# Optimization experiments

Hardware: AMD Instinct MI355X
Metric: run time of the kernel (lower is better)

The kernel has to match this reference:

```python
import jax, jax.numpy as jnp
import numpy as np
import math

B, S, D, H, DFF = 4, 1024, 1024, 16, 4096
DK = D // H
EPS = 1e-5


def setup_inputs() -> dict:
    key = jax.random.key(0)
    ks = jax.random.split(key, 20)
    n = lambda k, shp: jax.random.normal(k, shp, jnp.float32) * 0.02
    inp = {
        "x": jax.random.normal(ks[0], (B, S, D), jnp.float32),
        "enc_output": jax.random.normal(ks[1], (B, S, D), jnp.float32),
        # source_mask is unused by the module's forward; target_mask is causal
        "source_mask": jnp.ones((B, 1, 1, S), jnp.int32),
        "target_mask": jnp.tril(jnp.ones((1, 1, S, S), jnp.int32)),
        # self-attention (torch Linear: y = x @ W.T + b)
        "sa_wq": n(ks[2], (D, D)), "sa_bq": jnp.zeros((D,), jnp.float32),
        "sa_wk": n(ks[3], (D, D)), "sa_bk": jnp.zeros((D,), jnp.float32),
        "sa_wv": n(ks[4], (D, D)), "sa_bv": jnp.zeros((D,), jnp.float32),
        "sa_wo": n(ks[5], (D, D)), "sa_bo": jnp.zeros((D,), jnp.float32),
        # cross-attention (nn.MultiheadAttention packed in_proj)
        "ca_in_w": n(ks[6], (3 * D, D)), "ca_in_b": jnp.zeros((3 * D,), jnp.float32),
        "ca_out_w": n(ks[7], (D, D)), "ca_out_b": jnp.zeros((D,), jnp.float32),
        # feed-forward
        "ff_w1": n(ks[8], (DFF, D)), "ff_b1": jnp.zeros((DFF,), jnp.float32),
        "ff_w2": n(ks[9], (D, DFF)), "ff_b2": jnp.zeros((D,), jnp.float32),
        # layer norms
        "n1_g": jnp.ones((D,), jnp.float32), "n1_b": jnp.zeros((D,), jnp.float32),
        "n2_g": jnp.ones((D,), jnp.float32), "n2_b": jnp.zeros((D,), jnp.float32),
        "n3_g": jnp.ones((D,), jnp.float32), "n3_b": jnp.zeros((D,), jnp.float32),
    }
    return inp


def _layernorm(x, g, b):
    m = jnp.mean(x, axis=-1, keepdims=True)
    v = jnp.var(x, axis=-1, keepdims=True)
    return (x - m) * jax.lax.rsqrt(v + EPS) * g + b


def _split_heads(t):  # [B,L,D] -> [B,H,L,DK]
    Bb, L, _ = t.shape
    return t.reshape(Bb, L, H, DK).transpose(0, 2, 1, 3)


def _attn(q, k, v, mask):
    # q,k,v: [B,H,Lq/ Lk, DK]
    scores = jnp.einsum("bhqd,bhkd->bhqk", q, k) / math.sqrt(DK)
    if mask is not None:
        scores = jnp.where(mask == 0, jnp.float32(-1e9), scores)
    probs = jax.nn.softmax(scores, axis=-1)
    out = jnp.einsum("bhqk,bhkd->bhqd", probs, v)  # [B,H,Lq,DK]
    Bb, _, Lq, _ = out.shape
    return out.transpose(0, 2, 1, 3).reshape(Bb, Lq, D)


def reference(x, enc_output, source_mask, target_mask,
              sa_wq, sa_bq, sa_wk, sa_bk, sa_wv, sa_bv, sa_wo, sa_bo,
              ca_in_w, ca_in_b, ca_out_w, ca_out_b,
              ff_w1, ff_b1, ff_w2, ff_b2,
              n1_g, n1_b, n2_g, n2_b, n3_g, n3_b):
    # --- masked causal self-attention (hand-rolled MultiHeadAttention) ---
    q = _split_heads(x @ sa_wq.T + sa_bq)
    k = _split_heads(x @ sa_wk.T + sa_bk)
    v = _split_heads(x @ sa_wv.T + sa_bv)
    sa = _attn(q, k, v, target_mask) @ sa_wo.T + sa_bo
    x = _layernorm(x + sa, n1_g, n1_b)  # dropout p=0 -> identity

    # --- cross-attention (nn.MultiheadAttention, batch_first, no mask) ---
    wq, wk, wv = ca_in_w[:D], ca_in_w[D:2 * D], ca_in_w[2 * D:]
    bq, bk, bv = ca_in_b[:D], ca_in_b[D:2 * D], ca_in_b[2 * D:]
    q = _split_heads(x @ wq.T + bq)
    k = _split_heads(enc_output @ wk.T + bk)
    v = _split_heads(enc_output @ wv.T + bv)
    ca = _attn(q, k, v, None) @ ca_out_w.T + ca_out_b
    x = _layernorm(x + ca, n2_g, n2_b)

    # --- feed-forward ---
    ff = jax.nn.relu(x @ ff_w1.T + ff_b1) @ ff_w2.T + ff_b2
    x = _layernorm(x + ff, n3_g, n3_b)
    return x
```

## Files before the change

### kernel.cpp

```cpp
#include <hip/hip_runtime.h>
#include <hip/hip_bf16.h>
#include <stdint.h>
#include <math.h>

#define DEV static __device__ __forceinline__

typedef short bf16x8 __attribute__((ext_vector_type(8)));
typedef float f32x4 __attribute__((ext_vector_type(4)));
typedef float f32x16 __attribute__((ext_vector_type(16)));
typedef unsigned short u16;

static constexpr int Sq   = 1024;
static constexpr int Dm   = 1024;
static constexpr int Hh   = 16;
static constexpr int Mrows = 4096;
static constexpr int DFFn = 4096;


DEV u16 f2bf(float f) {
    union { float f; unsigned u; } c; c.f = f;
    unsigned u = c.u;
    return (u16)((u + 0x7FFFu + ((u >> 16) & 1u)) >> 16);
}

DEV float bf2f(u16 v) {
    union { unsigned u; float f; } c; c.u = ((unsigned)v) << 16; return c.f;
}

DEV unsigned cvt_pk_bf16(float lo, float hi) {
    unsigned r;
    asm("v_cvt_pk_bf16_f32 %0, %1, %2" : "=v"(r) : "v"(lo), "v"(hi));
    return r;
}

DEV float fast_exp2(float x) {
#if __has_builtin(__builtin_amdgcn_exp2f)
    return __builtin_amdgcn_exp2f(x);
#else
    float r; asm("v_exp_f32 %0, %1" : "=v"(r) : "v"(x)); return r;
#endif
}

DEV void gload_lds16(void* lds, const void* g) {
    using gvp = __attribute__((address_space(1))) void*;
    using lvp = __attribute__((address_space(3))) void*;
    __builtin_amdgcn_global_load_lds((gvp)const_cast<void*>(g), (lvp)lds, 16, 0, 0);
}

DEV int swz64(int L) { return L ^ (((L >> 7) & 7) << 4); }


__global__ __launch_bounds__(256) void cast_multi_kernel(
    const float* s0, const float* s1, const float* s2, const float* s3, const float* s4,
    const float* s5, const float* s6, const float* s7, const float* s8, const float* s9,
    u16* d0, u16* d1, u16* d2, u16* d3, u16* d4,
    u16* d5, u16* d6, u16* d7, u16* d8, u16* d9,
    int e0, int e1, int e2, int e3, int e4,
    int e5, int e6, int e7, int e8, int e9)
{
    int i = blockIdx.x * 256 + threadIdx.x;
    if (i >= e9) return;
    const float* s; u16* d; int b;
    if      (i < e0) { s = s0; d = d0; b = 0;  }
    else if (i < e1) { s = s1; d = d1; b = e0; }
    else if (i < e2) { s = s2; d = d2; b = e1; }
    else if (i < e3) { s = s3; d = d3; b = e2; }
    else if (i < e4) { s = s4; d = d4; b = e3; }
    else if (i < e5) { s = s5; d = d5; b = e4; }
    else if (i < e6) { s = s6; d = d6; b = e5; }
    else if (i < e7) { s = s7; d = d7; b = e6; }
    else if (i < e8) { s = s8; d = d8; b = e7; }
    else             { s = s9; d = d9; b = e8; }
    int j = i - b;
    float4 v = ((const float4*)s)[j];
    ushort4 o;
    o.x = f2bf(v.x); o.y = f2bf(v.y); o.z = f2bf(v.z); o.w = f2bf(v.w);
    ((ushort4*)d)[j] = o;
}


template<int MODE, int BSPLIT>
__global__ __launch_bounds__(512) void gemm256_kernel(
    const u16* __restrict__ A, const u16* __restrict__ W,
    const float* __restrict__ bias0, const float* __restrict__ bias1,
    const float* __restrict__ bias2,
    void* __restrict__ Cout,
    void* __restrict__ P1, void* __restrict__ P2, void* __restrict__ P3,
    int N, int ldK, int Kpass)
{
    __shared__ char ldsA[65536];
    __shared__ char ldsB[65536];
    const int tid = threadIdx.x;
    const int w = tid >> 6, l = tid & 63;
    const int lr = l & 15, lg = l >> 4;
    const int wr = w >> 2, wc = w & 3;

    const int nwg = gridDim.x * gridDim.y;
    const int lin = blockIdx.y * gridDim.x + blockIdx.x;
    const int swz = (lin & 7) * (nwg >> 3) + (lin >> 3);
    const size_t tm = (size_t)(swz / gridDim.x) * 256;
    const size_t tn = (size_t)(swz % gridDim.x) * 256;
    const size_t kz = (size_t)blockIdx.z * Kpass;

    int offA[8], offB[4];
    #pragma unroll
    for (int m = 0; m < 8; ++m)
        offA[m] = swz64((wr * 128 + m * 16 + lr) * 64 + lg * 16);
    #pragma unroll
    for (int n = 0; n < 4; ++n)
        offB[n] = swz64((wc * 64 + n * 16 + lr) * 64 + lg * 16);

    const int Ls = swz64(tid * 16);
    const int sr = Ls >> 6, scc = Ls & 63;
    const size_t ldb = (size_t)ldK * 2;
    const char* aS = (const char*)A + (tm + sr) * ldb + kz * 2 + scc;
    const char* bS = (const char*)W + (tn + sr) * ldb + kz * 2 + scc;

    auto AH = [&](int b, int h) -> char* { return ldsA + (b * 2 + h) * 16384; };
    auto BH = [&](int b, int h) -> char* { return ldsB + (b * 2 + h) * 16384; };
    auto stage = [&](char* half, const char* src) {
        gload_lds16(half + w * 1024, src);
        gload_lds16(half + 8192 + w * 1024, src + 128 * ldb);
    };

    const int nt = Kpass >> 6;
    const int niter = nt >> 1;

    f32x4 acc[8][4] = {};
    bf16x8 bq[4];

    stage(AH(0, 0), aS);        stage(BH(0, 0), bS);
    stage(AH(0, 1), aS + 64);   stage(BH(0, 1), bS + 64);
    stage(AH(1, 0), aS + 128);  stage(BH(1, 0), bS + 128);
    asm volatile("s_waitcnt vmcnt(4)" ::: "memory");
    __builtin_amdgcn_s_barrier();

    for (int it = 0; it < niter; ++it) {
        const int t0 = it * 2;
        const bool last = (it == niter - 1);
        #pragma unroll
        for (int p = 0; p < 8; ++p) {
            const int ts = p >> 2;
            const int kk = (p >> 1) & 1, mh = p & 1;

            if (mh == 0) {
                #pragma unroll
                for (int n = 0; n < 4; ++n)
                    bq[n] = *(const bf16x8*)(BH(ts, kk) + offB[n]);
            }
            bf16x8 aF[4];
            #pragma unroll
            for (int q = 0; q < 4; ++q)
                aF[q] = *(const bf16x8*)(AH(ts, kk) + offA[mh * 4 + q]);

            if (p == 0)      { stage(AH(1, 1), aS + (size_t)(t0 + 1) * 128 + 64); }
            else if (p == 1) { stage(BH(1, 1), bS + (size_t)(t0 + 1) * 128 + 64); }
            else if (p == 2) { if (t0 + 2 < nt) stage(AH(0, 0), aS + (size_t)(t0 + 2) * 128); }
            else if (p == 3) { if (t0 + 2 < nt) stage(BH(0, 0), bS + (size_t)(t0 + 2) * 128); }
            else if (p == 4) { if (t0 + 2 < nt) stage(AH(0, 1), aS + (size_t)(t0 + 2) * 128 + 64); }
            else if (p == 5) { if (t0 + 2 < nt) stage(BH(0, 1), bS + (size_t)(t0 + 2) * 128 + 64); }
            else if (p == 6) { if (t0 + 3 < nt) stage(AH(1, 0), aS + (size_t)(t0 + 3) * 128); }
            else             { if (t0 + 3 < nt) stage(BH(1, 0), bS + (size_t)(t0 + 3) * 128); }

            if (p == 3) {
                if (last) asm volatile("s_waitcnt vmcnt(0)" ::: "memory");
                else      asm volatile("s_waitcnt vmcnt(4)" ::: "memory");
            } else if (p == 7 && !last) {
                asm volatile("s_waitcnt vmcnt(4)" ::: "memory");
            }
            __builtin_amdgcn_s_barrier();
            asm volatile("s_waitcnt lgkmcnt(0)");
            __builtin_amdgcn_sched_barrier(0);
            __builtin_amdgcn_s_setprio(1);
            #pragma unroll
            for (int q = 0; q < 4; ++q)
                #pragma unroll
                for (int n = 0; n < 4; ++n)
                    acc[mh * 4 + q][n] = __builtin_amdgcn_mfma_f32_16x16x32_bf16(
                        aF[q], bq[n], acc[mh * 4 + q][n], 0, 0, 0);
            __builtin_amdgcn_s_setprio(0);
        }
    }

    u16* Pp = nullptr;
    float bv[4];
    if (MODE == 3) {
        Pp = (u16*)((blockIdx.z == 0) ? Cout : (blockIdx.z == 1) ? P1 : (blockIdx.z == 2) ? P2 : P3);
    } else {
        #pragma unroll
        for (int n = 0; n < 4; ++n) {
            const int col = (int)tn + wc * 64 + n * 16 + lr;
            if (BSPLIT) {
                const float* bp = (col < 1024) ? bias0 : (col < 2048) ? bias1 : bias2;
                bv[n] = bp[col & 1023];
            } else {
                bv[n] = bias0[col];
            }
        }
    }
    #pragma unroll
    for (int m = 0; m < 8; ++m) {
        #pragma unroll
        for (int n = 0; n < 4; ++n) {
            const size_t col = tn + wc * 64 + n * 16 + lr;
            #pragma unroll
            for (int j = 0; j < 4; ++j) {
                const size_t row = tm + wr * 128 + m * 16 + lg * 4 + j;
                if (MODE == 3) {
                    Pp[row * (size_t)N + col] = f2bf(acc[m][n][j]);
                } else {
                    float v = acc[m][n][j] + bv[n];
                    if (MODE == 2) v = fmaxf(v, 0.f);
                    ((u16*)Cout)[row * (size_t)N + col] = f2bf(v);
                }
            }
        }
    }
}


template<int OUT_BF16, int RELU, int BSPLIT>
__global__ __launch_bounds__(256, 3) void gemm_bt64_kernel(
    const u16* __restrict__ A, const u16* __restrict__ W,
    const float* __restrict__ bias0, const float* __restrict__ bias1,
    const float* __restrict__ bias2,
    void* __restrict__ Cout,
    int N, int K)
{
    __shared__ char Ald[2][8192];
    __shared__ char Bld[2][16384];
    const int tid = threadIdx.x;
    const int w  = tid >> 6, l = tid & 63;
    const int lr = l & 15,  lg = l >> 4;

    const int nwg = gridDim.x * gridDim.y;
    const int lin = blockIdx.y * gridDim.x + blockIdx.x;
    const int swz = (lin & 7) * (nwg >> 3) + (lin >> 3);
    const size_t tm = (size_t)(swz / gridDim.x) * 64;
    const size_t tn = (size_t)(swz % gridDim.x) * 128;

    const int Ls = swz64(tid * 16);
    const int sr = Ls >> 7, sc = (Ls & 127) >> 1;
    const u16* As = A + (tm + sr) * (size_t)K + sc;
    const u16* Bs = W + (tn + sr) * (size_t)K + sc;
    const int woff = w * 1024;

    auto stage = [&](int b, int k0) {
        gload_lds16(Ald[b] + woff,         As + k0);
        gload_lds16(Ald[b] + 4096 + woff,  As + (size_t)32 * K + k0);
        gload_lds16(Bld[b] + woff,         Bs + k0);
        gload_lds16(Bld[b] + 4096 + woff,  Bs + (size_t)32 * K + k0);
        gload_lds16(Bld[b] + 8192 + woff,  Bs + (size_t)64 * K + k0);
        gload_lds16(Bld[b] + 12288 + woff, Bs + (size_t)96 * K + k0);
    };

    int offA[4][2], offB[2][2];
    #pragma unroll
    for (int m = 0; m < 4; ++m)
        #pragma unroll
        for (int kk = 0; kk < 2; ++kk)
            offA[m][kk] = swz64((m * 16 + lr) * 128 + kk * 64 + lg * 16);
    #pragma unroll
    for (int n = 0; n < 2; ++n)
        #pragma unroll
        for (int kk = 0; kk < 2; ++kk)
            offB[n][kk] = swz64((w * 32 + n * 16 + lr) * 128 + kk * 64 + lg * 16);

    f32x4 acc[4][2] = {};
    const int nt = K >> 6;

    stage(0, 0);
    asm volatile("s_waitcnt vmcnt(0)" ::: "memory");
    __syncthreads();

    for (int t = 0; t < nt; ++t) {
        const int cur = t & 1;
        if (t + 1 < nt) stage(cur ^ 1, (t + 1) * 64);
        #pragma unroll
        for (int kk = 0; kk < 2; ++kk) {
            bf16x8 aF[4], bq[2];
            #pragma unroll
            for (int m = 0; m < 4; ++m) aF[m] = *(const bf16x8*)(Ald[cur] + offA[m][kk]);
            #pragma unroll
            for (int n = 0; n < 2; ++n) bq[n] = *(const bf16x8*)(Bld[cur] + offB[n][kk]);
            asm volatile("s_waitcnt lgkmcnt(0)");
            __builtin_amdgcn_sched_barrier(0);
            __builtin_amdgcn_s_setprio(1);
            #pragma unroll
            for (int m = 0; m < 4; ++m)
                #pragma unroll
                for (int n = 0; n < 2; ++n)
                    acc[m][n] = __builtin_amdgcn_mfma_f32_16x16x32_bf16(aF[m], bq[n], acc[m][n], 0, 0, 0);
            __builtin_amdgcn_s_setprio(0);
        }
        if (t + 1 < nt) asm volatile("s_waitcnt vmcnt(0)" ::: "memory");
        __syncthreads();
    }

    float bv[2];
    #pragma unroll
    for (int n = 0; n < 2; ++n) {
        const int col = (int)tn + w * 32 + n * 16 + lr;
        if (BSPLIT) {
            const float* bp = (col < 1024) ? bias0 : (col < 2048) ? bias1 : bias2;
            bv[n] = bp[col & 1023];
        } else {
            bv[n] = bias0[col];
        }
    }

    #pragma unroll
    for (int m = 0; m < 4; ++m) {
        #pragma unroll
        for (int n = 0; n < 2; ++n) {
            const size_t col = tn + w * 32 + n * 16 + lr;
            #pragma unroll
            for (int j = 0; j < 4; ++j) {
                const size_t row = tm + m * 16 + lg * 4 + j;
                float v = acc[m][n][j] + bv[n];
                if (RELU) v = fmaxf(v, 0.f);
                if (OUT_BF16) ((u16*)Cout)[row * (size_t)N + col] = f2bf(v);
                else          ((float*)Cout)[row * (size_t)N + col] = v;
            }
        }
    }
}


template<int CAUSAL>
__global__ __launch_bounds__(512, 2) void attn_kernel(
    const u16* __restrict__ Qm, int ldq,
    const u16* __restrict__ Km, int ldk,
    const u16* __restrict__ Vm, int ldv,
    u16* __restrict__ Om)
{
    __shared__ char lds[66048];

    const int tid = threadIdx.x;
    const int w = tid >> 6, l = tid & 63;
    const int lq = l & 31, hi = l >> 5;
    const int s = w & 3, hfk = w >> 2;
    const int bh = blockIdx.x;
    const int b = bh >> 4, h = bh & 15;
    const int q0 = (CAUSAL ? (gridDim.y - 1 - blockIdx.y) : blockIdx.y) * 128;
    const int qw0 = q0 + s * 32;
    const size_t baseQ = (size_t)b * Sq * ldq + (size_t)h * 64;
    const size_t baseK = (size_t)b * Sq * ldk + (size_t)h * 64;
    const size_t baseV = (size_t)b * Sq * ldv + (size_t)h * 64;
    const size_t baseO = (size_t)b * Sq * Dm  + (size_t)h * 64;

    const int qrow = qw0 + lq;
    bf16x8 bq[4];
    #pragma unroll
    for (int kc = 0; kc < 4; ++kc)
        bq[kc] = *(const bf16x8*)&Qm[baseQ + (size_t)qrow * ldq + kc * 16 + hi * 8];

    const int tl = tid & 255, pstg = tid >> 8;
    const int kr  = tl >> 2;
    const int kcB = (tl & 3) * 32;
    const int vdg = tl >> 5;
    const int vkp = tl & 31;

    f32x16 o0 = {}, o1 = {};
    float lj = 0.f;

    const int nt_blk  = CAUSAL ? ((q0 + 128) >> 6) : (Sq >> 6);
    const int nrounds = nt_blk >> 1;
    const float cexp = 0.125f * 1.44269504f;
    const float CSH  = 10.0f;

    uint4 ka, kb, va, vb;
    auto loadKV = [&](int rv) {
        const int kv = (rv * 2 + pstg) << 6;
        ka = *(const uint4*)&Km[baseK + (size_t)(kv + kr) * ldk + kcB / 2];
        kb = *(const uint4*)&Km[baseK + (size_t)(kv + kr) * ldk + kcB / 2 + 8];
        va = *(const uint4*)&Vm[baseV + (size_t)(kv + vkp * 2    ) * ldv + vdg * 8];
        vb = *(const uint4*)&Vm[baseV + (size_t)(kv + vkp * 2 + 1) * ldv + vdg * 8];
    };
    auto stageTo = [&](int bsel) {
        char* Kst = lds + bsel * 32768 + pstg * 8192;
        char* Vst = lds + bsel * 32768 + 16384 + pstg * 8192;
        const int sk = (kr & 7) << 4;
        *(uint4*)(Kst + kr * 128 + ((kcB     ) ^ sk)) = ka;
        *(uint4*)(Kst + kr * 128 + ((kcB + 16) ^ sk)) = kb;
        const u16* pa_ = (const u16*)&va;
        const u16* pb_ = (const u16*)&vb;
        #pragma unroll
        for (int i = 0; i < 8; ++i) {
            const int d = vdg * 8 + i;
            unsigned val = (unsigned)pa_[i] | ((unsigned)pb_[i] << 16);
            *(unsigned*)(Vst + d * 128 + ((vkp * 4) ^ ((d & 7) << 4))) = val;
        }
    };

    loadKV(0);
    stageTo(0);
    loadKV(1);
    __syncthreads();

    for (int r = 0; r < nrounds; ++r) {
        const int rp = r & 1;
        const char* Kb_ = lds + rp * 32768 + hfk * 8192;
        const char* Vb_ = lds + rp * 32768 + 16384 + hfk * 8192;
        const int kv0 = (r * 2 + hfk) << 6;
        const bool docmp = (!CAUSAL || kv0 < qw0 + 32);
        const int skq = (lq & 7) << 4;

        f32x16 sv[2];
        if (docmp) {
            sv[0] = (f32x16){}; sv[1] = (f32x16){};
            #pragma unroll
            for (int n = 0; n < 2; ++n) {
                const int rowb = (n * 32 + lq) * 128;
                #pragma unroll
                for (int kc = 0; kc < 4; ++kc) {
                    bf16x8 kf = *(const bf16x8*)(Kb_ + rowb + ((kc * 32 + hi * 16) ^ skq));
                    sv[n] = __builtin_amdgcn_mfma_f32_32x32x16_bf16(kf, bq[kc], sv[n], 0, 0, 0);
                }
            }
        }

        if (r + 1 < nrounds) stageTo(rp ^ 1);
        if (r + 2 < nrounds) loadKV(r + 2);

        if (docmp) {
            const bool diag = CAUSAL && (kv0 + 63 > qw0);
            float rs0 = 0.f, rs1 = 0.f;
            #pragma unroll
            for (int n = 0; n < 2; ++n)
                #pragma unroll
                for (int r2 = 0; r2 < 16; ++r2) {
                    float v = sv[n][r2];
                    if (diag) {
                        int key = kv0 + n * 32 + (r2 & 3) + 8 * (r2 >> 2) + 4 * hi;
                        if (key > qrow) v = -3.0e8f;
                    }
                    float e = fast_exp2(fmaf(v, cexp, -CSH));
                    sv[n][r2] = e;
                    if (r2 & 1) rs1 += e; else rs0 += e;
                }
            float rs = rs0 + rs1;
            rs += __shfl_xor(rs, 32);
            lj += rs;

            unsigned wv[2][8];
            #pragma unroll
            for (int n = 0; n < 2; ++n)
                #pragma unroll
                for (int m = 0; m < 8; ++m)
                    wv[n][m] = cvt_pk_bf16(sv[n][2 * m], sv[n][2 * m + 1]);

            #pragma unroll
            for (int ks = 0; ks < 4; ++ks) {
                const int n = ks >> 1, q_ = (ks & 1) * 4;
                unsigned r0 = (unsigned)__shfl_xor((int)wv[n][q_ + 0], 32);
                unsigned r1 = (unsigned)__shfl_xor((int)wv[n][q_ + 1], 32);
                unsigned r2w = (unsigned)__shfl_xor((int)wv[n][q_ + 2], 32);
                unsigned r3 = (unsigned)__shfl_xor((int)wv[n][q_ + 3], 32);
                union { unsigned u[4]; bf16x8 v; } pa;
                pa.u[0] = hi ? r2w           : wv[n][q_ + 0];
                pa.u[1] = hi ? r3            : wv[n][q_ + 1];
                pa.u[2] = hi ? wv[n][q_ + 2] : r0;
                pa.u[3] = hi ? wv[n][q_ + 3] : r1;
                const int koff = (ks * 32 + hi * 16);
                bf16x8 vf0 = *(const bf16x8*)(Vb_ + lq * 128        + (koff ^ skq));
                bf16x8 vf1 = *(const bf16x8*)(Vb_ + (32 + lq) * 128 + (koff ^ skq));
                o0 = __builtin_amdgcn_mfma_f32_32x32x16_bf16(pa.v, vf0, o0, 0, 0, 0);
                o1 = __builtin_amdgcn_mfma_f32_32x32x16_bf16(pa.v, vf1, o1, 0, 0, 0);
            }
        }
        __syncthreads();
    }

    char* ob = lds + s * 8192 + l * 128;
    float* mlb = (float*)(lds + 65536) + s * 32 + lq;
    const int sko = (l & 7) << 4;

    if (hfk == 1) {
        #pragma unroll
        for (int i = 0; i < 4; ++i) {
            f32x4 t0v = { o0[4 * i], o0[4 * i + 1], o0[4 * i + 2], o0[4 * i + 3] };
            f32x4 t1v = { o1[4 * i], o1[4 * i + 1], o1[4 * i + 2], o1[4 * i + 3] };
            *(f32x4*)(ob + ((i * 16) ^ sko))      = t0v;
            *(f32x4*)(ob + ((64 + i * 16) ^ sko)) = t1v;
        }
        if (hi == 0) mlb[0] = lj;
    }
    __syncthreads();
    if (hfk == 0) {
        const float linv = __builtin_amdgcn_rcpf(lj + mlb[0]);
        f32x4 b0[4], b1[4];
        #pragma unroll
        for (int i = 0; i < 4; ++i) {
            b0[i] = *(const f32x4*)(ob + ((i * 16) ^ sko));
            b1[i] = *(const f32x4*)(ob + ((64 + i * 16) ^ sko));
        }
        #pragma unroll
        for (int r2 = 0; r2 < 16; ++r2) {
            const int crow = (r2 & 3) + 8 * (r2 >> 2) + 4 * hi;
            const float lr_ = __shfl(linv, crow);
            const size_t rowoff = baseO + (size_t)(qw0 + crow) * Dm;
            float v0 = (o0[r2] + b0[r2 >> 2][r2 & 3]) * lr_;
            float v1 = (o1[r2] + b1[r2 >> 2][r2 & 3]) * lr_;
            Om[rowoff + lq]      = f2bf(v0);
            Om[rowoff + 32 + lq] = f2bf(v1);
        }
    }
}


__global__ __launch_bounds__(256) void add_ln_kernel(
    const u16* __restrict__ A, const u16* __restrict__ Bv,
    const float* __restrict__ g, const float* __restrict__ be,
    u16* __restrict__ Y)
{
    const int row = blockIdx.x;
    const int tid = threadIdx.x;
    const size_t off = (size_t)row * Dm;
    ushort4 a4 = ((const ushort4*)(A + off))[tid];
    ushort4 b4 = ((const ushort4*)(Bv + off))[tid];
    float4 xv;
    xv.x = bf2f(a4.x) + bf2f(b4.x);
    xv.y = bf2f(a4.y) + bf2f(b4.y);
    xv.z = bf2f(a4.z) + bf2f(b4.z);
    xv.w = bf2f(a4.w) + bf2f(b4.w);
    float s = xv.x + xv.y + xv.z + xv.w;
    float q = xv.x * xv.x + xv.y * xv.y + xv.z * xv.z + xv.w * xv.w;
    #pragma unroll
    for (int m = 1; m < 64; m <<= 1) {
        s += __shfl_xor(s, m);
        q += __shfl_xor(q, m);
    }
    __shared__ float ss[4], qq[4];
    if ((tid & 63) == 0) { ss[tid >> 6] = s; qq[tid >> 6] = q; }
    __syncthreads();
    s = ss[0] + ss[1] + ss[2] + ss[3];
    q = qq[0] + qq[1] + qq[2] + qq[3];
    const float mean = s * (1.f / 1024.f);
    const float var  = q * (1.f / 1024.f) - mean * mean;
    const float rstd = rsqrtf(var + 1e-5f);
    float4 g4  = ((const float4*)g)[tid];
    float4 be4 = ((const float4*)be)[tid];
    ushort4 ob;
    ob.x = f2bf((xv.x - mean) * rstd * g4.x + be4.x);
    ob.y = f2bf((xv.y - mean) * rstd * g4.y + be4.y);
    ob.z = f2bf((xv.z - mean) * rstd * g4.z + be4.z);
    ob.w = f2bf((xv.w - mean) * rstd * g4.w + be4.w);
    ((ushort4*)(Y + off))[tid] = ob;
}


__global__ __launch_bounds__(256) void add_ln_red4_kernel(
    const u16* __restrict__ X,
    const u16* __restrict__ P0, const u16* __restrict__ P1,
    const u16* __restrict__ P2, const u16* __restrict__ P3,
    const float* __restrict__ bias,
    const float* __restrict__ g, const float* __restrict__ be,
    float* __restrict__ Y)
{
    const int row = blockIdx.x;
    const int tid = threadIdx.x;
    const size_t off = (size_t)row * Dm;
    ushort4 a4 = ((const ushort4*)(X + off))[tid];
    ushort4 u0 = ((const ushort4*)(P0 + off))[tid];
    ushort4 u1 = ((const ushort4*)(P1 + off))[tid];
    ushort4 u2 = ((const ushort4*)(P2 + off))[tid];
    ushort4 u3 = ((const ushort4*)(P3 + off))[tid];
    float4 b4 = ((const float4*)bias)[tid];
    float4 xv;
    xv.x = bf2f(a4.x) + bf2f(u0.x) + bf2f(u1.x) + bf2f(u2.x) + bf2f(u3.x) + b4.x;
    xv.y = bf2f(a4.y) + bf2f(u0.y) + bf2f(u1.y) + bf2f(u2.y) + bf2f(u3.y) + b4.y;
    xv.z = bf2f(a4.z) + bf2f(u0.z) + bf2f(u1.z) + bf2f(u2.z) + bf2f(u3.z) + b4.z;
    xv.w = bf2f(a4.w) + bf2f(u0.w) + bf2f(u1.w) + bf2f(u2.w) + bf2f(u3.w) + b4.w;
    float s = xv.x + xv.y + xv.z + xv.w;
    float q = xv.x * xv.x + xv.y * xv.y + xv.z * xv.z + xv.w * xv.w;
    #pragma unroll
    for (int m = 1; m < 64; m <<= 1) {
        s += __shfl_xor(s, m);
        q += __shfl_xor(q, m);
    }
    __shared__ float ss[4], qq[4];
    if ((tid & 63) == 0) { ss[tid >> 6] = s; qq[tid >> 6] = q; }
    __syncthreads();
    s = ss[0] + ss[1] + ss[2] + ss[3];
    q = qq[0] + qq[1] + qq[2] + qq[3];
    const float mean = s * (1.f / 1024.f);
    const float var  = q * (1.f / 1024.f) - mean * mean;
    const float rstd = rsqrtf(var + 1e-5f);
    float4 g4  = ((const float4*)g)[tid];
    float4 be4 = ((const float4*)be)[tid];
    float4 y;
    y.x = (xv.x - mean) * rstd * g4.x + be4.x;
    y.y = (xv.y - mean) * rstd * g4.y + be4.y;
    y.z = (xv.z - mean) * rstd * g4.z + be4.z;
    y.w = (xv.w - mean) * rstd * g4.w + be4.w;
    ((float4*)(Y + off))[tid] = y;
}


extern "C" void kernel_launch(void* const* d_in, const int* in_sizes, int n_in,
                              void* d_out, int out_size, void* d_ws, size_t ws_size,
                              hipStream_t stream)
{
    const float* x       = (const float*)d_in[0];
    const float* enc     = (const float*)d_in[1];
    const float* sa_wq   = (const float*)d_in[4];
    const float* sa_bq   = (const float*)d_in[5];
    const float* sa_wk   = (const float*)d_in[6];
    const float* sa_bk   = (const float*)d_in[7];
    const float* sa_wv   = (const float*)d_in[8];
    const float* sa_bv   = (const float*)d_in[9];
    const float* sa_wo   = (const float*)d_in[10];
    const float* sa_bo   = (const float*)d_in[11];
    const float* ca_in_w = (const float*)d_in[12];
    const float* ca_in_b = (const float*)d_in[13];
    const float* ca_out_w= (const float*)d_in[14];
    const float* ca_out_b= (const float*)d_in[15];
    const float* ff_w1   = (const float*)d_in[16];
    const float* ff_b1   = (const float*)d_in[17];
    const float* ff_w2   = (const float*)d_in[18];
    const float* ff_b2   = (const float*)d_in[19];
    const float* n1_g = (const float*)d_in[20];
    const float* n1_b = (const float*)d_in[21];
    const float* n2_g = (const float*)d_in[22];
    const float* n2_b = (const float*)d_in[23];
    const float* n3_g = (const float*)d_in[24];
    const float* n3_b = (const float*)d_in[25];

    char* p = (char*)d_ws;
    auto take = [&](size_t bytes) -> char* {
        char* r = p; p += (bytes + 255) & ~(size_t)255; return r;
    };
    const size_t MDbf = (size_t)Mrows * Dm * 2;
    const size_t DD   = (size_t)Dm * Dm;

    u16* xb     = (u16*)take(MDbf);
    u16* encb   = (u16*)take(MDbf);
    u16* wqkv   = (u16*)take(3 * DD * 2);
    u16* wob    = (u16*)take(DD * 2);
    u16* cainb  = (u16*)take(3 * DD * 2);
    u16* caoutb = (u16*)take(DD * 2);
    u16* fw1b   = (u16*)take((size_t)DFFn * Dm * 2);
    u16* fw2b   = (u16*)take((size_t)Dm * DFFn * 2);
    u16* SCR    = (u16*)take((size_t)Mrows * DFFn * 2);
    u16* AOb    = (u16*)take(MDbf);
    u16* tmpb   = (u16*)take(MDbf);
    u16* x1bf   = (u16*)take(MDbf);
    u16* x2bf   = (u16*)take(MDbf);
    if ((size_t)(p - (char*)d_ws) > ws_size) return;

    u16* fp0 = AOb;
    u16* fp1 = tmpb;
    u16* fp2 = xb;
    u16* fp3 = encb;

    {
        const int sx  = (int)((size_t)Mrows * Dm / 4);
        const int sw  = (int)(DD / 4);
        const int e0 = sx;
        const int e1 = e0 + sx;
        const int e2 = e1 + sw;
        const int e3 = e2 + sw;
        const int e4 = e3 + sw;
        const int e5 = e4 + sw;
        const int e6 = e5 + 3 * sw;
        const int e7 = e6 + sw;
        const int e8 = e7 + 4 * sw;
        const int e9 = e8 + 4 * sw;
        cast_multi_kernel<<<dim3((e9 + 255) / 256), dim3(256), 0, stream>>>(
            x, enc, sa_wq, sa_wk, sa_wv, sa_wo, ca_in_w, ca_out_w, ff_w1, ff_w2,
            xb, encb, wqkv, wqkv + DD, wqkv + 2 * DD, wob, cainb, caoutb, fw1b, fw2b,
            e0, e1, e2, e3, e4, e5, e6, e7, e8, e9);
    }

    const dim3 blk(256);
    const dim3 blk512(512);
    const size_t M4 = (size_t)Mrows * Dm;

    gemm_bt64_kernel<1, 0, 1><<<dim3(3072 / 128, Mrows / 64), blk, 0, stream>>>(
        xb, wqkv, sa_bq, sa_bk, sa_bv, (void*)SCR, 3072, Dm);
    attn_kernel<1><<<dim3(4 * Hh, Sq / 128), blk512, 0, stream>>>(SCR, 3072, SCR + 1024, 3072, SCR + 2048, 3072, AOb);
    gemm_bt64_kernel<1, 0, 0><<<dim3(Dm / 128, Mrows / 64), blk, 0, stream>>>(
        AOb, wob, sa_bo, nullptr, nullptr, (void*)tmpb, Dm, Dm);
    add_ln_kernel<<<dim3(Mrows), blk, 0, stream>>>(xb, tmpb, n1_g, n1_b, x1bf);

    u16* Qc  = SCR;
    u16* KVc = SCR + M4;
    gemm_bt64_kernel<1, 0, 0><<<dim3(Dm / 128, Mrows / 64), blk, 0, stream>>>(
        x1bf, cainb, ca_in_b, nullptr, nullptr, (void*)Qc, Dm, Dm);
    gemm_bt64_kernel<1, 0, 0><<<dim3(2048 / 128, Mrows / 64), blk, 0, stream>>>(
        encb, cainb + DD, ca_in_b + Dm, nullptr, nullptr, (void*)KVc, 2048, Dm);
    attn_kernel<0><<<dim3(4 * Hh, Sq / 128), blk512, 0, stream>>>(Qc, 1024, KVc, 2048, KVc + 1024, 2048, AOb);
    gemm_bt64_kernel<1, 0, 0><<<dim3(Dm / 128, Mrows / 64), blk, 0, stream>>>(
        AOb, caoutb, ca_out_b, nullptr, nullptr, (void*)tmpb, Dm, Dm);
    add_ln_kernel<<<dim3(Mrows), blk, 0, stream>>>(x1bf, tmpb, n2_g, n2_b, x2bf);

    u16* ffh = SCR;
    gemm_bt64_kernel<1, 1, 0><<<dim3(DFFn / 128, Mrows / 64), blk, 0, stream>>>(
        x2bf, fw1b, ff_b1, nullptr, nullptr, (void*)ffh, DFFn, Dm);
    gemm256_kernel<3, 0><<<dim3(4, 16, 4), blk512, 0, stream>>>(
        ffh, fw2b, nullptr, nullptr, nullptr, (void*)fp0, (void*)fp1, (void*)fp2, (void*)fp3, Dm, DFFn, 1024);
    add_ln_red4_kernel<<<dim3(Mrows), blk, 0, stream>>>(x2bf, fp0, fp1, fp2, fp3, ff_b2, n3_g, n3_b, (float*)d_out);
}
```

Baseline: 310.0 us.

## Route QKV, cross-KV and FFN1 GEMMs through 256-tile kernel with split-K

```diff
diff --git a/kernel.cpp b/kernel.cpp
--- a/kernel.cpp
+++ b/kernel.cpp
@@ -76,6 +76,24 @@
     ushort4 o;
     o.x = f2bf(v.x); o.y = f2bf(v.y); o.z = f2bf(v.z); o.w = f2bf(v.w);
     ((ushort4*)d)[j] = o;
+}
+
+
+__global__ __launch_bounds__(256) void add2_bias_bf16_kernel(
+    const u16* __restrict__ P0, const u16* __restrict__ P1,
+    const float* __restrict__ bias, u16* __restrict__ Y, int N)
+{
+    const int i = blockIdx.x * 256 + threadIdx.x;
+    ushort4 a = ((const ushort4*)P0)[i];
+    ushort4 b = ((const ushort4*)P1)[i];
+    const int col = (i * 4) & (N - 1);
+    float4 bv = *(const float4*)&bias[col];
+    ushort4 o;
+    o.x = f2bf(bf2f(a.x) + bf2f(b.x) + bv.x);
+    o.y = f2bf(bf2f(a.y) + bf2f(b.y) + bv.y);
+    o.z = f2bf(bf2f(a.z) + bf2f(b.z) + bv.z);
+    o.w = f2bf(bf2f(a.w) + bf2f(b.w) + bv.w);
+    ((ushort4*)Y)[i] = o;
 }
 
 
@@ -647,12 +665,16 @@
     u16* tmpb   = (u16*)take(MDbf);
     u16* x1bf   = (u16*)take(MDbf);
     u16* x2bf   = (u16*)take(MDbf);
+    u16* cpbuf  = (u16*)take((size_t)Mrows * 2048 * 2);
     if ((size_t)(p - (char*)d_ws) > ws_size) return;
 
     u16* fp0 = AOb;
     u16* fp1 = tmpb;
     u16* fp2 = xb;
     u16* fp3 = encb;
+
+    u16* cp0 = cpbuf;
+    u16* cp1 = AOb;
 
     {
         const int sx  = (int)((size_t)Mrows * Dm / 4);
@@ -677,8 +699,8 @@
     const dim3 blk512(512);
     const size_t M4 = (size_t)Mrows * Dm;
 
-    gemm_bt64_kernel<1, 0, 1><<<dim3(3072 / 128, Mrows / 64), blk, 0, stream>>>(
-        xb, wqkv, sa_bq, sa_bk, sa_bv, (void*)SCR, 3072, Dm);
+    gemm256_kernel<1, 1><<<dim3(12, 16), blk512, 0, stream>>>(
+        xb, wqkv, sa_bq, sa_bk, sa_bv, (void*)SCR, nullptr, nullptr, nullptr, 3072, Dm, Dm);
     attn_kernel<1><<<dim3(4 * Hh, Sq / 128), blk512, 0, stream>>>(SCR, 3072, SCR + 1024, 3072, SCR + 2048, 3072, AOb);
     gemm_bt64_kernel<1, 0, 0><<<dim3(Dm / 128, Mrows / 64), blk, 0, stream>>>(
         AOb, wob, sa_bo, nullptr, nullptr, (void*)tmpb, Dm, Dm);
@@ -688,16 +710,19 @@
     u16* KVc = SCR + M4;
     gemm_bt64_kernel<1, 0, 0><<<dim3(Dm / 128, Mrows / 64), blk, 0, stream>>>(
         x1bf, cainb, ca_in_b, nullptr, nullptr, (void*)Qc, Dm, Dm);
-    gemm_bt64_kernel<1, 0, 0><<<dim3(2048 / 128, Mrows / 64), blk, 0, stream>>>(
-        encb, cainb + DD, ca_in_b + Dm, nullptr, nullptr, (void*)KVc, 2048, Dm);
+    gemm256_kernel<3, 0><<<dim3(8, 16, 2), blk512, 0, stream>>>(
+        encb, cainb + DD, nullptr, nullptr, nullptr,
+        (void*)cp0, (void*)cp1, nullptr, nullptr, 2048, Dm, 512);
+    add2_bias_bf16_kernel<<<dim3((Mrows * 2048 / 4) / 256), blk, 0, stream>>>(
+        cp0, cp1, ca_in_b + Dm, KVc, 2048);
     attn_kernel<0><<<dim3(4 * Hh, Sq / 128), blk512, 0, stream>>>(Qc, 1024, KVc, 2048, KVc + 1024, 2048, AOb);
     gemm_bt64_kernel<1, 0, 0><<<dim3(Dm / 128, Mrows / 64), blk, 0, stream>>>(
         AOb, caoutb, ca_out_b, nullptr, nullptr, (void*)tmpb, Dm, Dm);
     add_ln_kernel<<<dim3(Mrows), blk, 0, stream>>>(x1bf, tmpb, n2_g, n2_b, x2bf);
 
     u16* ffh = SCR;
-    gemm_bt64_kernel<1, 1, 0><<<dim3(DFFn / 128, Mrows / 64), blk, 0, stream>>>(
-        x2bf, fw1b, ff_b1, nullptr, nullptr, (void*)ffh, DFFn, Dm);
+    gemm256_kernel<2, 0><<<dim3(16, 16), blk512, 0, stream>>>(
+        x2bf, fw1b, ff_b1, ff_b1, ff_b1, (void*)ffh, nullptr, nullptr, nullptr, DFFn, Dm, Dm);
     gemm256_kernel<3, 0><<<dim3(4, 16, 4), blk512, 0, stream>>>(
         ffh, fw2b, nullptr, nullptr, nullptr, (void*)fp0, (void*)fp1, (void*)fp2, (void*)fp3, Dm, DFFn, 1024);
     add_ln_red4_kernel<<<dim3(Mrows), blk, 0, stream>>>(x2bf, fp0, fp1, fp2, fp3, ff_b2, n3_g, n3_b, (float*)d_out);
```

New measurement: 290.9 us. 1.07x faster.

## Route large projection GEMMs to 256-tile kernel and restructure its inner loop

Applied to the files above, without the earlier changes.

```diff
diff --git a/kernel.cpp b/kernel.cpp
--- a/kernel.cpp
+++ b/kernel.cpp
@@ -127,7 +127,6 @@
     const int niter = nt >> 1;
 
     f32x4 acc[8][4] = {};
-    bf16x8 bq[4];
 
     stage(AH(0, 0), aS);        stage(BH(0, 0), bS);
     stage(AH(0, 1), aS + 64);   stage(BH(0, 1), bS + 64);
@@ -139,33 +138,42 @@
         const int t0 = it * 2;
         const bool last = (it == niter - 1);
         #pragma unroll
-        for (int p = 0; p < 8; ++p) {
-            const int ts = p >> 2;
-            const int kk = (p >> 1) & 1, mh = p & 1;
-
-            if (mh == 0) {
-                #pragma unroll
-                for (int n = 0; n < 4; ++n)
-                    bq[n] = *(const bf16x8*)(BH(ts, kk) + offB[n]);
+        for (int q = 0; q < 4; ++q) {
+            const int ts = q >> 1;
+            const int kk = q & 1;
+
+            bf16x8 bqv[4], aF[8];
+            #pragma unroll
+            for (int n = 0; n < 4; ++n)
+                bqv[n] = *(const bf16x8*)(BH(ts, kk) + offB[n]);
+            #pragma unroll
+            for (int m = 0; m < 8; ++m)
+                aF[m] = *(const bf16x8*)(AH(ts, kk) + offA[m]);
+
+            if (q == 0) {
+                stage(AH(1, 1), aS + (size_t)(t0 + 1) * 128 + 64);
+                stage(BH(1, 1), bS + (size_t)(t0 + 1) * 128 + 64);
+            } else if (q == 1) {
+                if (t0 + 2 < nt) {
+                    stage(AH(0, 0), aS + (size_t)(t0 + 2) * 128);
+                    stage(BH(0, 0), bS + (size_t)(t0 + 2) * 128);
+                }
+            } else if (q == 2) {
+                if (t0 + 2 < nt) {
+                    stage(AH(0, 1), aS + (size_t)(t0 + 2) * 128 + 64);
+                    stage(BH(0, 1), bS + (size_t)(t0 + 2) * 128 + 64);
+                }
+            } else {
+                if (t0 + 3 < nt) {
+                    stage(AH(1, 0), aS + (size_t)(t0 + 3) * 128);
+                    stage(BH(1, 0), bS + (size_t)(t0 + 3) * 128);
+                }
             }
-            bf16x8 aF[4];
-            #pragma unroll
-            for (int q = 0; q < 4; ++q)
-                aF[q] = *(const bf16x8*)(AH(ts, kk) + offA[mh * 4 + q]);
-
-            if (p == 0)      { stage(AH(1, 1), aS + (size_t)(t0 + 1) * 128 + 64); }
-            else if (p == 1) { stage(BH(1, 1), bS + (size_t)(t0 + 1) * 128 + 64); }
-            else if (p == 2) { if (t0 + 2 < nt) stage(AH(0, 0), aS + (size_t)(t0 + 2) * 128); }
-            else if (p == 3) { if (t0 + 2 < nt) stage(BH(0, 0), bS + (size_t)(t0 + 2) * 128); }
-            else if (p == 4) { if (t0 + 2 < nt) stage(AH(0, 1), aS + (size_t)(t0 + 2) * 128 + 64); }
-            else if (p == 5) { if (t0 + 2 < nt) stage(BH(0, 1), bS + (size_t)(t0 + 2) * 128 + 64); }
-            else if (p == 6) { if (t0 + 3 < nt) stage(AH(1, 0), aS + (size_t)(t0 + 3) * 128); }
-            else             { if (t0 + 3 < nt) stage(BH(1, 0), bS + (size_t)(t0 + 3) * 128); }
-
-            if (p == 3) {
+
+            if (q == 1) {
                 if (last) asm volatile("s_waitcnt vmcnt(0)" ::: "memory");
                 else      asm volatile("s_waitcnt vmcnt(4)" ::: "memory");
-            } else if (p == 7 && !last) {
+            } else if (q == 3 && !last) {
                 asm volatile("s_waitcnt vmcnt(4)" ::: "memory");
             }
             __builtin_amdgcn_s_barrier();
@@ -173,11 +181,11 @@
             __builtin_amdgcn_sched_barrier(0);
             __builtin_amdgcn_s_setprio(1);
             #pragma unroll
-            for (int q = 0; q < 4; ++q)
+            for (int m = 0; m < 8; ++m)
                 #pragma unroll
                 for (int n = 0; n < 4; ++n)
-                    acc[mh * 4 + q][n] = __builtin_amdgcn_mfma_f32_16x16x32_bf16(
-                        aF[q], bq[n], acc[mh * 4 + q][n], 0, 0, 0);
+                    acc[m][n] = __builtin_amdgcn_mfma_f32_16x16x32_bf16(
+                        aF[m], bqv[n], acc[m][n], 0, 0, 0);
             __builtin_amdgcn_s_setprio(0);
         }
     }
@@ -677,8 +685,8 @@
     const dim3 blk512(512);
     const size_t M4 = (size_t)Mrows * Dm;
 
-    gemm_bt64_kernel<1, 0, 1><<<dim3(3072 / 128, Mrows / 64), blk, 0, stream>>>(
-        xb, wqkv, sa_bq, sa_bk, sa_bv, (void*)SCR, 3072, Dm);
+    gemm256_kernel<1, 1><<<dim3(12, 16), blk512, 0, stream>>>(
+        xb, wqkv, sa_bq, sa_bk, sa_bv, (void*)SCR, nullptr, nullptr, nullptr, 3072, Dm, Dm);
     attn_kernel<1><<<dim3(4 * Hh, Sq / 128), blk512, 0, stream>>>(SCR, 3072, SCR + 1024, 3072, SCR + 2048, 3072, AOb);
     gemm_bt64_kernel<1, 0, 0><<<dim3(Dm / 128, Mrows / 64), blk, 0, stream>>>(
         AOb, wob, sa_bo, nullptr, nullptr, (void*)tmpb, Dm, Dm);
@@ -688,16 +696,17 @@
     u16* KVc = SCR + M4;
     gemm_bt64_kernel<1, 0, 0><<<dim3(Dm / 128, Mrows / 64), blk, 0, stream>>>(
         x1bf, cainb, ca_in_b, nullptr, nullptr, (void*)Qc, Dm, Dm);
-    gemm_bt64_kernel<1, 0, 0><<<dim3(2048 / 128, Mrows / 64), blk, 0, stream>>>(
-        encb, cainb + DD, ca_in_b + Dm, nullptr, nullptr, (void*)KVc, 2048, Dm);
+    gemm256_kernel<1, 1><<<dim3(8, 16), blk512, 0, stream>>>(
+        encb, cainb + DD, ca_in_b + Dm, ca_in_b + 2 * Dm, ca_in_b + 2 * Dm,
+        (void*)KVc, nullptr, nullptr, nullptr, 2048, Dm, Dm);
     attn_kernel<0><<<dim3(4 * Hh, Sq / 128), blk512, 0, stream>>>(Qc, 1024, KVc, 2048, KVc + 1024, 2048, AOb);
     gemm_bt64_kernel<1, 0, 0><<<dim3(Dm / 128, Mrows / 64), blk, 0, stream>>>(
         AOb, caoutb, ca_out_b, nullptr, nullptr, (void*)tmpb, Dm, Dm);
     add_ln_kernel<<<dim3(Mrows), blk, 0, stream>>>(x1bf, tmpb, n2_g, n2_b, x2bf);
 
     u16* ffh = SCR;
-    gemm_bt64_kernel<1, 1, 0><<<dim3(DFFn / 128, Mrows / 64), blk, 0, stream>>>(
-        x2bf, fw1b, ff_b1, nullptr, nullptr, (void*)ffh, DFFn, Dm);
+    gemm256_kernel<2, 0><<<dim3(16, 16), blk512, 0, stream>>>(
+        x2bf, fw1b, ff_b1, ff_b1, ff_b1, (void*)ffh, nullptr, nullptr, nullptr, DFFn, Dm, Dm);
     gemm256_kernel<3, 0><<<dim3(4, 16, 4), blk512, 0, stream>>>(
         ffh, fw2b, nullptr, nullptr, nullptr, (void*)fp0, (void*)fp1, (void*)fp2, (void*)fp3, Dm, DFFn, 1024);
     add_ln_red4_kernel<<<dim3(Mrows), blk, 0, stream>>>(x2bf, fp0, fp1, fp2, fp3, ff_b2, n3_g, n3_b, (float*)d_out);
```

New measurement: 306.2 us. Within noise of the previous version (-1.2%).

## Fuse self-attn QKV and cross-attn KV projections into one 256-tile GEMM launch

Applied to the files above, without the earlier changes.

```diff
diff --git a/kernel.cpp b/kernel.cpp
--- a/kernel.cpp
+++ b/kernel.cpp
@@ -79,6 +79,103 @@
 }
 
 
+struct G256State {
+    f32x4 acc[8][4];
+};
+
+template<typename EPI>
+DEV void g256_body(const u16* A, const u16* W, size_t tm, size_t tn, size_t kz,
+                   int ldK, int Kpass, int tid, EPI&& epilogue,
+                   char* ldsA, char* ldsB)
+{
+    const int w = tid >> 6, l = tid & 63;
+    const int lr = l & 15, lg = l >> 4;
+    const int wr = w >> 2, wc = w & 3;
+
+    int offA[8], offB[4];
+    #pragma unroll
+    for (int m = 0; m < 8; ++m)
+        offA[m] = swz64((wr * 128 + m * 16 + lr) * 64 + lg * 16);
+    #pragma unroll
+    for (int n = 0; n < 4; ++n)
+        offB[n] = swz64((wc * 64 + n * 16 + lr) * 64 + lg * 16);
+
+    const int Ls = swz64(tid * 16);
+    const int sr = Ls >> 6, scc = Ls & 63;
+    const size_t ldb = (size_t)ldK * 2;
+    const char* aS = (const char*)A + (tm + sr) * ldb + kz * 2 + scc;
+    const char* bS = (const char*)W + (tn + sr) * ldb + kz * 2 + scc;
+
+    auto AH = [&](int b, int h) -> char* { return ldsA + (b * 2 + h) * 16384; };
+    auto BH = [&](int b, int h) -> char* { return ldsB + (b * 2 + h) * 16384; };
+    auto stage = [&](char* half, const char* src) {
+        gload_lds16(half + w * 1024, src);
+        gload_lds16(half + 8192 + w * 1024, src + 128 * ldb);
+    };
+
+    const int nt = Kpass >> 6;
+    const int niter = nt >> 1;
+
+    f32x4 acc[8][4] = {};
+    bf16x8 bq[4];
+
+    stage(AH(0, 0), aS);        stage(BH(0, 0), bS);
+    stage(AH(0, 1), aS + 64);   stage(BH(0, 1), bS + 64);
+    stage(AH(1, 0), aS + 128);  stage(BH(1, 0), bS + 128);
+    asm volatile("s_waitcnt vmcnt(4)" ::: "memory");
+    __builtin_amdgcn_s_barrier();
+
+    for (int it = 0; it < niter; ++it) {
+        const int t0 = it * 2;
+        const bool last = (it == niter - 1);
+        #pragma unroll
+        for (int p = 0; p < 8; ++p) {
+            const int ts = p >> 2;
+            const int kk = (p >> 1) & 1, mh = p & 1;
+
+            if (mh == 0) {
+                #pragma unroll
+                for (int n = 0; n < 4; ++n)
+                    bq[n] = *(const bf16x8*)(BH(ts, kk) + offB[n]);
+            }
+            bf16x8 aF[4];
+            #pragma unroll
+            for (int q = 0; q < 4; ++q)
+                aF[q] = *(const bf16x8*)(AH(ts, kk) + offA[mh * 4 + q]);
+
+            if (p == 0)      { stage(AH(1, 1), aS + (size_t)(t0 + 1) * 128 + 64); }
+            else if (p == 1) { stage(BH(1, 1), bS + (size_t)(t0 + 1) * 128 + 64); }
+            else if (p == 2) { if (t0 + 2 < nt) stage(AH(0, 0), aS + (size_t)(t0 + 2) * 128); }
+            else if (p == 3) { if (t0 + 2 < nt) stage(BH(0, 0), bS + (size_t)(t0 + 2) * 128); }
+            else if (p == 4) { if (t0 + 2 < nt) stage(AH(0, 1), aS + (size_t)(t0 + 2) * 128 + 64); }
+            else if (p == 5) { if (t0 + 2 < nt) stage(BH(0, 1), bS + (size_t)(t0 + 2) * 128 + 64); }
+            else if (p == 6) { if (t0 + 3 < nt) stage(AH(1, 0), aS + (size_t)(t0 + 3) * 128); }
+            else             { if (t0 + 3 < nt) stage(BH(1, 0), bS + (size_t)(t0 + 3) * 128); }
+
+            if (p == 3) {
+                if (last) asm volatile("s_waitcnt vmcnt(0)" ::: "memory");
+                else      asm volatile("s_waitcnt vmcnt(4)" ::: "memory");
+            } else if (p == 7 && !last) {
+                asm volatile("s_waitcnt vmcnt(4)" ::: "memory");
+            }
+            __builtin_amdgcn_s_barrier();
+            asm volatile("s_waitcnt lgkmcnt(0)");
+            __builtin_amdgcn_sched_barrier(0);
+            __builtin_amdgcn_s_setprio(1);
+            #pragma unroll
+            for (int q = 0; q < 4; ++q)
+                #pragma unroll
+                for (int n = 0; n < 4; ++n)
+                    acc[mh * 4 + q][n] = __builtin_amdgcn_mfma_f32_16x16x32_bf16(
+                        aF[q], bq[n], acc[mh * 4 + q][n], 0, 0, 0);
+            __builtin_amdgcn_s_setprio(0);
+        }
+    }
+
+    epilogue(acc, wr, wc, lr, lg);
+}
+
+
 template<int MODE, int BSPLIT>
 __global__ __launch_bounds__(512) void gemm256_kernel(
     const u16* __restrict__ A, const u16* __restrict__ W,
@@ -91,9 +188,6 @@
     __shared__ char ldsA[65536];
     __shared__ char ldsB[65536];
     const int tid = threadIdx.x;
-    const int w = tid >> 6, l = tid & 63;
-    const int lr = l & 15, lg = l >> 4;
-    const int wr = w >> 2, wc = w & 3;
 
     const int nwg = gridDim.x * gridDim.y;
     const int lin = blockIdx.y * gridDim.x + blockIdx.x;
@@ -102,120 +196,94 @@
     const size_t tn = (size_t)(swz % gridDim.x) * 256;
     const size_t kz = (size_t)blockIdx.z * Kpass;
 
-    int offA[8], offB[4];
-    #pragma unroll
-    for (int m = 0; m < 8; ++m)
-        offA[m] = swz64((wr * 128 + m * 16 + lr) * 64 + lg * 16);
-    #pragma unroll
-    for (int n = 0; n < 4; ++n)
-        offB[n] = swz64((wc * 64 + n * 16 + lr) * 64 + lg * 16);
-
-    const int Ls = swz64(tid * 16);
-    const int sr = Ls >> 6, scc = Ls & 63;
-    const size_t ldb = (size_t)ldK * 2;
-    const char* aS = (const char*)A + (tm + sr) * ldb + kz * 2 + scc;
-    const char* bS = (const char*)W + (tn + sr) * ldb + kz * 2 + scc;
-
-    auto AH = [&](int b, int h) -> char* { return ldsA + (b * 2 + h) * 16384; };
-    auto BH = [&](int b, int h) -> char* { return ldsB + (b * 2 + h) * 16384; };
-    auto stage = [&](char* half, const char* src) {
-        gload_lds16(half + w * 1024, src);
-        gload_lds16(half + 8192 + w * 1024, src + 128 * ldb);
-    };
-
-    const int nt = Kpass >> 6;
-    const int niter = nt >> 1;
-
-    f32x4 acc[8][4] = {};
-    bf16x8 bq[4];
-
-    stage(AH(0, 0), aS);        stage(BH(0, 0), bS);
-    stage(AH(0, 1), aS + 64);   stage(BH(0, 1), bS + 64);
-    stage(AH(1, 0), aS + 128);  stage(BH(1, 0), bS + 128);
-    asm volatile("s_waitcnt vmcnt(4)" ::: "memory");
-    __builtin_amdgcn_s_barrier();
-
-    for (int it = 0; it < niter; ++it) {
-        const int t0 = it * 2;
-        const bool last = (it == niter - 1);
-        #pragma unroll
-        for (int p = 0; p < 8; ++p) {
-            const int ts = p >> 2;
-            const int kk = (p >> 1) & 1, mh = p & 1;
-
-            if (mh == 0) {
-                #pragma unroll
-                for (int n = 0; n < 4; ++n)
-                    bq[n] = *(const bf16x8*)(BH(ts, kk) + offB[n]);
-            }
-            bf16x8 aF[4];
-            #pragma unroll
-            for (int q = 0; q < 4; ++q)
-                aF[q] = *(const bf16x8*)(AH(ts, kk) + offA[mh * 4 + q]);
-
-            if (p == 0)      { stage(AH(1, 1), aS + (size_t)(t0 + 1) * 128 + 64); }
-            else if (p == 1) { stage(BH(1, 1), bS + (size_t)(t0 + 1) * 128 + 64); }
-            else if (p == 2) { if (t0 + 2 < nt) stage(AH(0, 0), aS + (size_t)(t0 + 2) * 128); }
-            else if (p == 3) { if (t0 + 2 < nt) stage(BH(0, 0), bS + (size_t)(t0 + 2) * 128); }
-            else if (p == 4) { if (t0 + 2 < nt) stage(AH(0, 1), aS + (size_t)(t0 + 2) * 128 + 64); }
-            else if (p == 5) { if (t0 + 2 < nt) stage(BH(0, 1), bS + (size_t)(t0 + 2) * 128 + 64); }
-            else if (p == 6) { if (t0 + 3 < nt) stage(AH(1, 0), aS + (size_t)(t0 + 3) * 128); }
-            else             { if (t0 + 3 < nt) stage(BH(1, 0), bS + (size_t)(t0 + 3) * 128); }
-
-            if (p == 3) {
-                if (last) asm volatile("s_waitcnt vmcnt(0)" ::: "memory");
-                else      asm volatile("s_waitcnt vmcnt(4)" ::: "memory");
-            } else if (p == 7 && !last) {
-                asm volatile("s_waitcnt vmcnt(4)" ::: "memory");
-            }
-            __builtin_amdgcn_s_barrier();
-            asm volatile("s_waitcnt lgkmcnt(0)");
-            __builtin_amdgcn_sched_barrier(0);
-            __builtin_amdgcn_s_setprio(1);
-            #pragma unroll
-            for (int q = 0; q < 4; ++q)
-                #pragma unroll
-                for (int n = 0; n < 4; ++n)
-                    acc[mh * 4 + q][n] = __builtin_amdgcn_mfma_f32_16x16x32_bf16(
-                        aF[q], bq[n], acc[mh * 4 + q][n], 0, 0, 0);
-            __builtin_amdgcn_s_setprio(0);
-        }
-    }
-
-    u16* Pp = nullptr;
-    float bv[4];
-    if (MODE == 3) {
-        Pp = (u16*)((blockIdx.z == 0) ? Cout : (blockIdx.z == 1) ? P1 : (blockIdx.z == 2) ? P2 : P3);
-    } else {
-        #pragma unroll
-        for (int n = 0; n < 4; ++n) {
-            const int col = (int)tn + wc * 64 + n * 16 + lr;
-            if (BSPLIT) {
-                const float* bp = (col < 1024) ? bias0 : (col < 2048) ? bias1 : bias2;
+    g256_body(A, W, tm, tn, kz, ldK, Kpass, tid,
+        [&](f32x4 (&acc)[8][4], int wr, int wc, int lr, int lg) {
+            u16* Pp = nullptr;
+            float bv[4];
+            if (MODE == 3) {
+                Pp = (u16*)((blockIdx.z == 0) ? Cout : (blockIdx.z == 1) ? P1 : (blockIdx.z == 2) ? P2 : P3);
+            } else {
+                #pragma unroll
+                for (int n = 0; n < 4; ++n) {
+                    const int col = (int)tn + wc * 64 + n * 16 + lr;
+                    if (BSPLIT) {
+                        const float* bp = (col < 1024) ? bias0 : (col < 2048) ? bias1 : bias2;
+                        bv[n] = bp[col & 1023];
+                    } else {
+                        bv[n] = bias0[col];
+                    }
+                }
+            }
+            #pragma unroll
+            for (int m = 0; m < 8; ++m) {
+                #pragma unroll
+                for (int n = 0; n < 4; ++n) {
+                    const size_t col = tn + wc * 64 + n * 16 + lr;
+                    #pragma unroll
+                    for (int j = 0; j < 4; ++j) {
+                        const size_t row = tm + wr * 128 + m * 16 + lg * 4 + j;
+                        if (MODE == 3) {
+                            Pp[row * (size_t)N + col] = f2bf(acc[m][n][j]);
+                        } else {
+                            float v = acc[m][n][j] + bv[n];
+                            if (MODE == 2) v = fmaxf(v, 0.f);
+                            ((u16*)Cout)[row * (size_t)N + col] = f2bf(v);
+                        }
+                    }
+                }
+            }
+        }, ldsA, ldsB);
+}
+
+
+__global__ __launch_bounds__(512) void gemm256_dual_kernel(
+    const u16* __restrict__ A0, const u16* __restrict__ W0, u16* __restrict__ C0,
+    const float* __restrict__ b0a, const float* __restrict__ b0b, const float* __restrict__ b0c,
+    const u16* __restrict__ A1, const u16* __restrict__ W1, u16* __restrict__ C1,
+    const float* __restrict__ b1a, const float* __restrict__ b1b)
+{
+    __shared__ char ldsA[65536];
+    __shared__ char ldsB[65536];
+    const int tid = threadIdx.x;
+
+    const int nwg = gridDim.x;
+    const int lin = blockIdx.x;
+    const int swz = (lin & 7) * (nwg >> 3) + (lin >> 3);
+
+    const bool seg0 = (swz < 192);
+    const int t = seg0 ? swz : (swz - 192);
+    const int gx = seg0 ? 12 : 8;
+    const int Np = seg0 ? 3072 : 2048;
+    const u16* A = seg0 ? A0 : A1;
+    const u16* W = seg0 ? W0 : W1;
+    u16* C = seg0 ? C0 : C1;
+    const size_t tm = (size_t)(t / gx) * 256;
+    const size_t tn = (size_t)(t % gx) * 256;
+
+    g256_body(A, W, tm, tn, 0, Dm, Dm, tid,
+        [&](f32x4 (&acc)[8][4], int wr, int wc, int lr, int lg) {
+            float bv[4];
+            #pragma unroll
+            for (int n = 0; n < 4; ++n) {
+                const int col = (int)tn + wc * 64 + n * 16 + lr;
+                const float* bp = seg0
+                    ? ((col < 1024) ? b0a : (col < 2048) ? b0b : b0c)
+                    : ((col < 1024) ? b1a : b1b);
                 bv[n] = bp[col & 1023];
-            } else {
-                bv[n] = bias0[col];
-            }
-        }
-    }
-    #pragma unroll
-    for (int m = 0; m < 8; ++m) {
-        #pragma unroll
-        for (int n = 0; n < 4; ++n) {
-            const size_t col = tn + wc * 64 + n * 16 + lr;
-            #pragma unroll
-            for (int j = 0; j < 4; ++j) {
-                const size_t row = tm + wr * 128 + m * 16 + lg * 4 + j;
-                if (MODE == 3) {
-                    Pp[row * (size_t)N + col] = f2bf(acc[m][n][j]);
-                } else {
-                    float v = acc[m][n][j] + bv[n];
-                    if (MODE == 2) v = fmaxf(v, 0.f);
-                    ((u16*)Cout)[row * (size_t)N + col] = f2bf(v);
+            }
+            #pragma unroll
+            for (int m = 0; m < 8; ++m) {
+                #pragma unroll
+                for (int n = 0; n < 4; ++n) {
+                    const size_t col = tn + wc * 64 + n * 16 + lr;
+                    #pragma unroll
+                    for (int j = 0; j < 4; ++j) {
+                        const size_t row = tm + wr * 128 + m * 16 + lg * 4 + j;
+                        C[row * (size_t)Np + col] = f2bf(acc[m][n][j] + bv[n]);
+                    }
                 }
             }
-        }
-    }
+        }, ldsA, ldsB);
 }
 
 
@@ -647,6 +715,7 @@
     u16* tmpb   = (u16*)take(MDbf);
     u16* x1bf   = (u16*)take(MDbf);
     u16* x2bf   = (u16*)take(MDbf);
+    u16* kvbuf  = (u16*)take((size_t)Mrows * 2048 * 2);
     if ((size_t)(p - (char*)d_ws) > ws_size) return;
 
     u16* fp0 = AOb;
@@ -675,29 +744,27 @@
 
     const dim3 blk(256);
     const dim3 blk512(512);
-    const size_t M4 = (size_t)Mrows * Dm;
-
-    gemm_bt64_kernel<1, 0, 1><<<dim3(3072 / 128, Mrows / 64), blk, 0, stream>>>(
-        xb, wqkv, sa_bq, sa_bk, sa_bv, (void*)SCR, 3072, Dm);
+
+    gemm256_dual_kernel<<<dim3(320), blk512, 0, stream>>>(
+        xb, wqkv, SCR, sa_bq, sa_bk, sa_bv,
+        encb, cainb + DD, kvbuf, ca_in_b + Dm, ca_in_b + 2 * Dm);
+
     attn_kernel<1><<<dim3(4 * Hh, Sq / 128), blk512, 0, stream>>>(SCR, 3072, SCR + 1024, 3072, SCR + 2048, 3072, AOb);
     gemm_bt64_kernel<1, 0, 0><<<dim3(Dm / 128, Mrows / 64), blk, 0, stream>>>(
         AOb, wob, sa_bo, nullptr, nullptr, (void*)tmpb, Dm, Dm);
     add_ln_kernel<<<dim3(Mrows), blk, 0, stream>>>(xb, tmpb, n1_g, n1_b, x1bf);
 
-    u16* Qc  = SCR;
-    u16* KVc = SCR + M4;
+    u16* Qc = SCR;
     gemm_bt64_kernel<1, 0, 0><<<dim3(Dm / 128, Mrows / 64), blk, 0, stream>>>(
         x1bf, cainb, ca_in_b, nullptr, nullptr, (void*)Qc, Dm, Dm);
-    gemm_bt64_kernel<1, 0, 0><<<dim3(2048 / 128, Mrows / 64), blk, 0, stream>>>(
-        encb, cainb + DD, ca_in_b + Dm, nullptr, nullptr, (void*)KVc, 2048, Dm);
-    attn_kernel<0><<<dim3(4 * Hh, Sq / 128), blk512, 0, stream>>>(Qc, 1024, KVc, 2048, KVc + 1024, 2048, AOb);
+    attn_kernel<0><<<dim3(4 * Hh, Sq / 128), blk512, 0, stream>>>(Qc, 1024, kvbuf, 2048, kvbuf + 1024, 2048, AOb);
     gemm_bt64_kernel<1, 0, 0><<<dim3(Dm / 128, Mrows / 64), blk, 0, stream>>>(
         AOb, caoutb, ca_out_b, nullptr, nullptr, (void*)tmpb, Dm, Dm);
     add_ln_kernel<<<dim3(Mrows), blk, 0, stream>>>(x1bf, tmpb, n2_g, n2_b, x2bf);
 
     u16* ffh = SCR;
-    gemm_bt64_kernel<1, 1, 0><<<dim3(DFFn / 128, Mrows / 64), blk, 0, stream>>>(
-        x2bf, fw1b, ff_b1, nullptr, nullptr, (void*)ffh, DFFn, Dm);
+    gemm256_kernel<2, 0><<<dim3(16, 16), blk512, 0, stream>>>(
+        x2bf, fw1b, ff_b1, ff_b1, ff_b1, (void*)ffh, nullptr, nullptr, nullptr, DFFn, Dm, Dm);
     gemm256_kernel<3, 0><<<dim3(4, 16, 4), blk512, 0, stream>>>(
         ffh, fw2b, nullptr, nullptr, nullptr, (void*)fp0, (void*)fp1, (void*)fp2, (void*)fp3, Dm, DFFn, 1024);
     add_ln_red4_kernel<<<dim3(Mrows), blk, 0, stream>>>(x2bf, fp0, fp1, fp2, fp3, ff_b2, n3_g, n3_b, (float*)d_out);
```

After: 284.4 us. 1.09x faster.
